# Kernel optimization log

Hardware: AMD Instinct MI355X
Metric: run time of the kernel (lower is better)

Reference implementation:

```python
import jax, jax.numpy as jnp
import numpy as np

EPS = 1e-5


def _rms_norm(x, w):
    # x: [..., C], w: [C]
    inv = jax.lax.rsqrt(jnp.mean(x * x, axis=-1, keepdims=True) + EPS)
    return x * inv * w


def setup_inputs() -> dict:
    key = jax.random.key(0)
    ks = jax.random.split(key, 8)
    N, H, C = 16384, 16, 32
    NE = 196608
    return {
        "q": jax.random.normal(ks[0], (N, H, C), dtype=jnp.float32),
        "k": jax.random.normal(ks[1], (N, H, C), dtype=jnp.float32),
        "v": jax.random.normal(ks[2], (N, H, C), dtype=jnp.float32),
        "e": jax.random.normal(ks[3], (NE, H, C), dtype=jnp.float32),
        "w_q_norm": jnp.ones((C,), dtype=jnp.float32),
        "w_k_norm": jnp.ones((C,), dtype=jnp.float32),
        "edge_src": jax.random.randint(ks[4], (NE,), 0, N, dtype=jnp.int32),
        "edge_dst": jax.random.randint(ks[5], (NE,), 0, N, dtype=jnp.int32),
    }


def reference(q, k, v, e, w_q_norm, w_k_norm, edge_src, edge_dst):
    N, H, C = q.shape
    qk_scale = 1.0 / np.sqrt(float(C))
    # fused QK RMSNorm (qk_norm == 1, elementwise_affine)
    qn = _rms_norm(q, w_q_norm)            # [N,H,C]
    kn = _rms_norm(k, w_k_norm)            # [N,H,C]
    ke = kn[edge_src] + e                  # [NE,H,C]
    ve = v[edge_src] + e                   # [NE,H,C]
    s = jnp.einsum("ehc,ehc->eh", qn[edge_dst], ke) * qk_scale  # [NE,H]
    # segment softmax over incoming edges per dst node
    m = jax.ops.segment_max(s, edge_dst, num_segments=N)        # [N,H]
    m = jnp.where(jnp.isfinite(m), m, 0.0)                      # empty rows -> 0 (matches kernel)
    alpha = jnp.exp(s - m[edge_dst])                            # [NE,H]
    denom = jax.ops.segment_sum(alpha, edge_dst, num_segments=N)            # [N,H]
    num = jax.ops.segment_sum(alpha[..., None] * ve, edge_dst, num_segments=N)  # [N,H,C]
    out = num / jnp.where(denom > 0, denom, 1.0)[..., None]
    return out
```

## Files before the change

kernel.cpp:

```cpp
#include <hip/hip_runtime.h>
#include <math.h>

#define H_DIM 16
#define C_DIM 32
#define HC_DIM (H_DIM * C_DIM)
#define EPSF 1e-5f

__device__ __forceinline__ float reduce8(float x) {
    x += __shfl_xor(x, 1);
    x += __shfl_xor(x, 2);
    x += __shfl_xor(x, 4);
    return x;
}

typedef float f4_raw __attribute__((ext_vector_type(4)));
__device__ __forceinline__ float4 nt_load4(const float* p) {
    f4_raw r = __builtin_nontemporal_load((const f4_raw*)p);
    return make_float4(r.x, r.y, r.z, r.w);
}
__device__ __forceinline__ void nt_store4(float* p, float4 v) {
    f4_raw r = {v.x, v.y, v.z, v.w};
    __builtin_nontemporal_store(r, (f4_raw*)p);
}

__global__ void zero_kernel(int* __restrict__ p, int n) {
    int i = blockIdx.x * blockDim.x + threadIdx.x;
    if (i < n) p[i] = 0;
}

__global__ void hist_kernel(const int* __restrict__ edst, int* __restrict__ counts, int ne) {
    int i = blockIdx.x * blockDim.x + threadIdx.x;
    if (i < ne) atomicAdd(&counts[edst[i]], 1);
}

__global__ void kinv_kernel(const float* __restrict__ k, float* __restrict__ kinv, int rows) {
    int gt = blockIdx.x * blockDim.x + threadIdx.x;
    int row = gt >> 3;
    if (row < rows) {
        const float4 kv = *(const float4*)(k + (size_t)row * C_DIM + ((gt & 7) << 2));
        float s = kv.x * kv.x + kv.y * kv.y + kv.z * kv.z + kv.w * kv.w;
        s = reduce8(s);
        if ((gt & 7) == 0) kinv[row] = rsqrtf(s * (1.0f / C_DIM) + EPSF);
    }
}

__global__ __launch_bounds__(1024)
void scan_kernel(const int* __restrict__ counts, int* __restrict__ offsets, int n) {
    __shared__ int wsum[16];
    __shared__ int carry_s;
    const int tid = threadIdx.x;
    const int lane = tid & 63;
    const int wid = tid >> 6;
    if (tid == 0) { carry_s = 0; offsets[0] = 0; }
    __syncthreads();
    for (int base = 0; base < n; base += 1024) {
        int x = (base + tid < n) ? counts[base + tid] : 0;
        int v = x;
        #pragma unroll
        for (int off = 1; off < 64; off <<= 1) {
            int y = __shfl_up(v, off);
            if (lane >= off) v += y;
        }
        if (lane == 63) wsum[wid] = v;
        __syncthreads();
        if (wid == 0 && lane < 16) {
            int s = wsum[lane];
            #pragma unroll
            for (int off = 1; off < 16; off <<= 1) {
                int y = __shfl_up(s, off);
                if (lane >= off) s += y;
            }
            wsum[lane] = s;
        }
        __syncthreads();
        int waveoff = (wid == 0) ? 0 : wsum[wid - 1];
        int carry = carry_s;
        if (base + tid < n) offsets[base + tid + 1] = carry + waveoff + v;
        __syncthreads();
        if (tid == 1023) carry_s = carry + wsum[15];
        __syncthreads();
    }
}

__global__ void scatter_kernel(const int* __restrict__ esrc, const int* __restrict__ edst,
                               const int* __restrict__ offsets, int* __restrict__ cursor,
                               int2* __restrict__ perm, int ne) {
    int i = blockIdx.x * blockDim.x + threadIdx.x;
    if (i < ne) {
        int d = edst[i];
        int pos = offsets[d] + atomicAdd(&cursor[d], 1);
        perm[pos] = make_int2(esrc[i], i);
    }
}

struct EdgeData {
    float4 ev, kv, vv;
    float  ki;
};

__device__ __forceinline__ EdgeData load_edge(int2 p,
                                              const float* __restrict__ e,
                                              const float* __restrict__ k,
                                              const float* __restrict__ v,
                                              const float* __restrict__ kinv,
                                              int hc, int h) {
    EdgeData d;
    d.ev = nt_load4(e + (size_t)p.y * HC_DIM + hc);
    d.kv = *(const float4*)(k + p.x * HC_DIM + hc);
    d.vv = *(const float4*)(v + p.x * HC_DIM + hc);
    d.ki = kinv[p.x * H_DIM + h];
    return d;
}

__device__ __forceinline__ void update_edge(const EdgeData& d,
                                            float4 qn, float4 wkv, float qk_scale,
                                            float& m, float& l, float4& acc) {
    float kex = d.kv.x * (d.ki * wkv.x) + d.ev.x;
    float key = d.kv.y * (d.ki * wkv.y) + d.ev.y;
    float kez = d.kv.z * (d.ki * wkv.z) + d.ev.z;
    float kew = d.kv.w * (d.ki * wkv.w) + d.ev.w;
    float dd = qn.x * kex + qn.y * key + qn.z * kez + qn.w * kew;
    dd = reduce8(dd);
    float s = dd * qk_scale;
    float mnew = fmaxf(m, s);
    float sc = __expf(m - mnew);
    float al = __expf(s - mnew);
    l = l * sc + al;
    acc.x = acc.x * sc + al * (d.vv.x + d.ev.x);
    acc.y = acc.y * sc + al * (d.vv.y + d.ev.y);
    acc.z = acc.z * sc + al * (d.vv.z + d.ev.z);
    acc.w = acc.w * sc + al * (d.vv.w + d.ev.w);
    m = mnew;
}

__global__ __launch_bounds__(128, 4)
void attn_kernel(const float* __restrict__ q, const float* __restrict__ k,
                 const float* __restrict__ v, const float* __restrict__ e,
                 const float* __restrict__ wq, const float* __restrict__ wk,
                 const float* __restrict__ kinv,
                 const int* __restrict__ offsets, const int2* __restrict__ perm,
                 float* __restrict__ out)
{
    const int node = blockIdx.x;
    const int t = threadIdx.x;
    const int hc = t << 2;
    const int c4 = (t & 7) << 2;
    const int h  = t >> 3;
    const float qk_scale = 0.17677669529663687f;

    const int node_off = node * HC_DIM + hc;

    float4 qv = *(const float4*)(q + node_off);
    float qs = qv.x * qv.x + qv.y * qv.y + qv.z * qv.z + qv.w * qv.w;
    qs = reduce8(qs);
    float qinv = rsqrtf(qs * (1.0f / C_DIM) + EPSF);
    float4 wqv = *(const float4*)(wq + c4);
    float4 qn = make_float4(qv.x * qinv * wqv.x, qv.y * qinv * wqv.y,
                            qv.z * qinv * wqv.z, qv.w * qinv * wqv.w);
    float4 wkv = *(const float4*)(wk + c4);

    const int row0 = offsets[node];
    const int row1 = offsets[node + 1];
    const int len = row1 - row0;
    const int mid = row0 + ((len + 1) >> 1);

    float mA = -INFINITY, lA = 0.0f, mB = -INFINITY, lB = 0.0f;
    float4 accA = make_float4(0.f, 0.f, 0.f, 0.f);
    float4 accB = make_float4(0.f, 0.f, 0.f, 0.f);

    int jA = row0, jB = mid;
    if (jB < row1) {
        int2 pA = perm[jA];
        int2 pB = perm[jB];
        EdgeData a = load_edge(pA, e, k, v, kinv, hc, h);
        EdgeData b = load_edge(pB, e, k, v, kinv, hc, h);
        ++jA; ++jB;
        bool haveNext = (jB < row1);
        int2 nA, nB;
        if (haveNext) { nA = perm[jA]; nB = perm[jB]; }
        while (haveNext) {
            EdgeData a2 = load_edge(nA, e, k, v, kinv, hc, h);
            EdgeData b2 = load_edge(nB, e, k, v, kinv, hc, h);
            ++jA; ++jB;
            haveNext = (jB < row1);
            if (haveNext) { nA = perm[jA]; nB = perm[jB]; }
            update_edge(a, qn, wkv, qk_scale, mA, lA, accA);
            update_edge(b, qn, wkv, qk_scale, mB, lB, accB);
            a = a2; b = b2;
        }
        update_edge(a, qn, wkv, qk_scale, mA, lA, accA);
        update_edge(b, qn, wkv, qk_scale, mB, lB, accB);
    }
    while (jA < mid) {
        int2 p = perm[jA];
        EdgeData a = load_edge(p, e, k, v, kinv, hc, h);
        update_edge(a, qn, wkv, qk_scale, mA, lA, accA);
        ++jA;
    }

    float M = fmaxf(mA, mB);
    float fA = (lA > 0.0f) ? __expf(mA - M) : 0.0f;
    float fB = (lB > 0.0f) ? __expf(mB - M) : 0.0f;
    float l = lA * fA + lB * fB;
    float4 acc = make_float4(accA.x * fA + accB.x * fB,
                             accA.y * fA + accB.y * fB,
                             accA.z * fA + accB.z * fB,
                             accA.w * fA + accB.w * fB);

    float invl = (l > 0.0f) ? (1.0f / l) : 0.0f;
    nt_store4(out + node_off, make_float4(acc.x * invl, acc.y * invl,
                                          acc.z * invl, acc.w * invl));
}

extern "C" void kernel_launch(void* const* d_in, const int* in_sizes, int n_in,
                              void* d_out, int out_size, void* d_ws, size_t ws_size,
                              hipStream_t stream) {
    const float* q  = (const float*)d_in[0];
    const float* k  = (const float*)d_in[1];
    const float* v  = (const float*)d_in[2];
    const float* e  = (const float*)d_in[3];
    const float* wq = (const float*)d_in[4];
    const float* wk = (const float*)d_in[5];
    const int* esrc = (const int*)d_in[6];
    const int* edst = (const int*)d_in[7];
    float* out = (float*)d_out;

    const int NE = in_sizes[6];
    const int HC = in_sizes[3] / NE;
    const int N  = in_sizes[0] / HC;

    int2* perm    = (int2*)d_ws;
    int* counts   = (int*)(perm + NE);
    int* cursor   = counts + N;
    int* offsets  = cursor + N;
    float* kinv   = (float*)(offsets + N + 1);

    const int rows = N * H_DIM;

    zero_kernel<<<(2 * N + 255) / 256, 256, 0, stream>>>(counts, 2 * N);
    hist_kernel<<<(NE + 255) / 256, 256, 0, stream>>>(edst, counts, NE);
    kinv_kernel<<<(rows * 8 + 255) / 256, 256, 0, stream>>>(k, kinv, rows);
    scan_kernel<<<1, 1024, 0, stream>>>(counts, offsets, N);
    scatter_kernel<<<(NE + 255) / 256, 256, 0, stream>>>(esrc, edst, offsets, cursor,
                                                         perm, NE);
    attn_kernel<<<N, 128, 0, stream>>>(q, k, v, e, wq, wk, kinv, offsets, perm, out);
}
```

Before: 696.4 us.

## Fuse histogram with k-norm, vectorize scan/scatter, fold scales into query

Merges the histogram and k-inverse-norm kernels into one launch and makes the histogram and scatter kernels handle four edges per thread with int4 loads. The scan now gives each thread 16 counts, cutting the loop to one iteration for 16384 nodes. In the attention kernel, the k-norm weight and qk scale are folded into precomputed query vectors, so each edge needs two dot products and no per-element key reconstruction. The q load is also marked nontemporal. The setup kernels are small next to the gather-bound attention kernel, so the combined effect is likely modest.

```diff
diff --git a/kernel.cpp b/kernel.cpp
--- a/kernel.cpp
+++ b/kernel.cpp
@@ -28,19 +28,30 @@
     if (i < n) p[i] = 0;
 }
 
-__global__ void hist_kernel(const int* __restrict__ edst, int* __restrict__ counts, int ne) {
-    int i = blockIdx.x * blockDim.x + threadIdx.x;
-    if (i < ne) atomicAdd(&counts[edst[i]], 1);
-}
-
-__global__ void kinv_kernel(const float* __restrict__ k, float* __restrict__ kinv, int rows) {
-    int gt = blockIdx.x * blockDim.x + threadIdx.x;
-    int row = gt >> 3;
-    if (row < rows) {
-        const float4 kv = *(const float4*)(k + (size_t)row * C_DIM + ((gt & 7) << 2));
-        float s = kv.x * kv.x + kv.y * kv.y + kv.z * kv.z + kv.w * kv.w;
-        s = reduce8(s);
-        if ((gt & 7) == 0) kinv[row] = rsqrtf(s * (1.0f / C_DIM) + EPSF);
+__global__ __launch_bounds__(256)
+void hist_kinv_kernel(const int* __restrict__ edst, int* __restrict__ counts,
+                      const float* __restrict__ k, float* __restrict__ kinv,
+                      int ne, int rows, int histBlocks) {
+    if ((int)blockIdx.x < histBlocks) {
+        int i4 = (blockIdx.x * 256 + threadIdx.x) * 4;
+        if (i4 + 4 <= ne) {
+            int4 d = *(const int4*)(edst + i4);
+            atomicAdd(&counts[d.x], 1);
+            atomicAdd(&counts[d.y], 1);
+            atomicAdd(&counts[d.z], 1);
+            atomicAdd(&counts[d.w], 1);
+        } else {
+            for (int j = i4; j < ne; ++j) atomicAdd(&counts[edst[j]], 1);
+        }
+    } else {
+        int gt = (blockIdx.x - histBlocks) * 256 + threadIdx.x;
+        int row = gt >> 3;
+        if (row < rows) {
+            const float4 kv = *(const float4*)(k + (size_t)row * C_DIM + ((gt & 7) << 2));
+            float s = kv.x * kv.x + kv.y * kv.y + kv.z * kv.z + kv.w * kv.w;
+            s = reduce8(s);
+            if ((gt & 7) == 0) kinv[row] = rsqrtf(s * (1.0f / C_DIM) + EPSF);
+        }
     }
 }
 
@@ -51,11 +62,26 @@
     const int tid = threadIdx.x;
     const int lane = tid & 63;
     const int wid = tid >> 6;
-    if (tid == 0) { carry_s = 0; offsets[0] = 0; }
+    if (tid == 0) carry_s = 0;
     __syncthreads();
-    for (int base = 0; base < n; base += 1024) {
-        int x = (base + tid < n) ? counts[base + tid] : 0;
-        int v = x;
+    for (int b0 = 0; b0 < n; b0 += 16384) {
+        const int base = b0 + tid * 16;
+        int c[16];
+        if (base + 16 <= n) {
+            const int4* p = (const int4*)(counts + base);
+            int4 t0 = p[0], t1 = p[1], t2 = p[2], t3 = p[3];
+            c[0]=t0.x; c[1]=t0.y; c[2]=t0.z; c[3]=t0.w;
+            c[4]=t1.x; c[5]=t1.y; c[6]=t1.z; c[7]=t1.w;
+            c[8]=t2.x; c[9]=t2.y; c[10]=t2.z; c[11]=t2.w;
+            c[12]=t3.x; c[13]=t3.y; c[14]=t3.z; c[15]=t3.w;
+        } else {
+            #pragma unroll
+            for (int j = 0; j < 16; ++j) c[j] = (base + j < n) ? counts[base + j] : 0;
+        }
+        int s = 0;
+        #pragma unroll
+        for (int j = 0; j < 16; ++j) s += c[j];
+        int v = s;
         #pragma unroll
         for (int off = 1; off < 64; off <<= 1) {
             int y = __shfl_up(v, off);
@@ -64,20 +90,34 @@
         if (lane == 63) wsum[wid] = v;
         __syncthreads();
         if (wid == 0 && lane < 16) {
-            int s = wsum[lane];
+            int w = wsum[lane];
             #pragma unroll
             for (int off = 1; off < 16; off <<= 1) {
-                int y = __shfl_up(s, off);
-                if (lane >= off) s += y;
+                int y = __shfl_up(w, off);
+                if (lane >= off) w += y;
             }
-            wsum[lane] = s;
+            wsum[lane] = w;
         }
         __syncthreads();
-        int waveoff = (wid == 0) ? 0 : wsum[wid - 1];
-        int carry = carry_s;
-        if (base + tid < n) offsets[base + tid + 1] = carry + waveoff + v;
+        const int carry = carry_s;
+        int p = carry + (wid ? wsum[wid - 1] : 0) + (v - s);
+        int o[16];
+        #pragma unroll
+        for (int j = 0; j < 16; ++j) { o[j] = p; p += c[j]; }
+        if (base + 16 <= n) {
+            int4* q = (int4*)(offsets + base);
+            q[0] = make_int4(o[0], o[1], o[2], o[3]);
+            q[1] = make_int4(o[4], o[5], o[6], o[7]);
+            q[2] = make_int4(o[8], o[9], o[10], o[11]);
+            q[3] = make_int4(o[12], o[13], o[14], o[15]);
+        } else {
+            #pragma unroll
+            for (int j = 0; j < 16; ++j)
+                if (base + j < n) offsets[base + j] = o[j];
+        }
+        if (n - 1 >= base && n - 1 < base + 16) offsets[n] = p;
         __syncthreads();
-        if (tid == 1023) carry_s = carry + wsum[15];
+        if (tid == 0) carry_s = carry + wsum[15];
         __syncthreads();
     }
 }
@@ -85,11 +125,24 @@
 __global__ void scatter_kernel(const int* __restrict__ esrc, const int* __restrict__ edst,
                                const int* __restrict__ offsets, int* __restrict__ cursor,
                                int2* __restrict__ perm, int ne) {
-    int i = blockIdx.x * blockDim.x + threadIdx.x;
-    if (i < ne) {
-        int d = edst[i];
-        int pos = offsets[d] + atomicAdd(&cursor[d], 1);
-        perm[pos] = make_int2(esrc[i], i);
+    int i4 = (blockIdx.x * blockDim.x + threadIdx.x) * 4;
+    if (i4 + 4 <= ne) {
+        int4 d = *(const int4*)(edst + i4);
+        int4 s = *(const int4*)(esrc + i4);
+        int p0 = offsets[d.x] + atomicAdd(&cursor[d.x], 1);
+        perm[p0] = make_int2(s.x, i4 + 0);
+        int p1 = offsets[d.y] + atomicAdd(&cursor[d.y], 1);
+        perm[p1] = make_int2(s.y, i4 + 1);
+        int p2 = offsets[d.z] + atomicAdd(&cursor[d.z], 1);
+        perm[p2] = make_int2(s.z, i4 + 2);
+        int p3 = offsets[d.w] + atomicAdd(&cursor[d.w], 1);
+        perm[p3] = make_int2(s.w, i4 + 3);
+    } else {
+        for (int j = i4; j < ne; ++j) {
+            int d = edst[j];
+            int pos = offsets[d] + atomicAdd(&cursor[d], 1);
+            perm[pos] = make_int2(esrc[j], j);
+        }
     }
 }
 
@@ -113,15 +166,11 @@
 }
 
 __device__ __forceinline__ void update_edge(const EdgeData& d,
-                                            float4 qn, float4 wkv, float qk_scale,
+                                            float4 qnw, float4 qns,
                                             float& m, float& l, float4& acc) {
-    float kex = d.kv.x * (d.ki * wkv.x) + d.ev.x;
-    float key = d.kv.y * (d.ki * wkv.y) + d.ev.y;
-    float kez = d.kv.z * (d.ki * wkv.z) + d.ev.z;
-    float kew = d.kv.w * (d.ki * wkv.w) + d.ev.w;
-    float dd = qn.x * kex + qn.y * key + qn.z * kez + qn.w * kew;
-    dd = reduce8(dd);
-    float s = dd * qk_scale;
+    float dk = qnw.x * d.kv.x + qnw.y * d.kv.y + qnw.z * d.kv.z + qnw.w * d.kv.w;
+    float de = qns.x * d.ev.x + qns.y * d.ev.y + qns.z * d.ev.z + qns.w * d.ev.w;
+    float s = reduce8(dk * d.ki + de);
     float mnew = fmaxf(m, s);
     float sc = __expf(m - mnew);
     float al = __expf(s - mnew);
@@ -150,14 +199,18 @@
 
     const int node_off = node * HC_DIM + hc;
 
-    float4 qv = *(const float4*)(q + node_off);
+    float4 qv = nt_load4(q + node_off);
     float qs = qv.x * qv.x + qv.y * qv.y + qv.z * qv.z + qv.w * qv.w;
     qs = reduce8(qs);
     float qinv = rsqrtf(qs * (1.0f / C_DIM) + EPSF);
     float4 wqv = *(const float4*)(wq + c4);
+    float4 wkv = *(const float4*)(wk + c4);
     float4 qn = make_float4(qv.x * qinv * wqv.x, qv.y * qinv * wqv.y,
                             qv.z * qinv * wqv.z, qv.w * qinv * wqv.w);
-    float4 wkv = *(const float4*)(wk + c4);
+    float4 qnw = make_float4(qn.x * wkv.x * qk_scale, qn.y * wkv.y * qk_scale,
+                             qn.z * wkv.z * qk_scale, qn.w * wkv.w * qk_scale);
+    float4 qns = make_float4(qn.x * qk_scale, qn.y * qk_scale,
+                             qn.z * qk_scale, qn.w * qk_scale);
 
     const int row0 = offsets[node];
     const int row1 = offsets[node + 1];
@@ -184,17 +237,17 @@
             ++jA; ++jB;
             haveNext = (jB < row1);
             if (haveNext) { nA = perm[jA]; nB = perm[jB]; }
-            update_edge(a, qn, wkv, qk_scale, mA, lA, accA);
-            update_edge(b, qn, wkv, qk_scale, mB, lB, accB);
+            update_edge(a, qnw, qns, mA, lA, accA);
+            update_edge(b, qnw, qns, mB, lB, accB);
             a = a2; b = b2;
         }
-        update_edge(a, qn, wkv, qk_scale, mA, lA, accA);
-        update_edge(b, qn, wkv, qk_scale, mB, lB, accB);
+        update_edge(a, qnw, qns, mA, lA, accA);
+        update_edge(b, qnw, qns, mB, lB, accB);
     }
     while (jA < mid) {
         int2 p = perm[jA];
         EdgeData a = load_edge(p, e, k, v, kinv, hc, h);
-        update_edge(a, qn, wkv, qk_scale, mA, lA, accA);
+        update_edge(a, qnw, qns, mA, lA, accA);
         ++jA;
     }
 
@@ -236,12 +289,15 @@
     float* kinv   = (float*)(offsets + N + 1);
 
     const int rows = N * H_DIM;
+    const int histBlocks = (NE / 4 + 255) / 256;
+    const int kinvBlocks = (rows * 8 + 255) / 256;
+    const int scatBlocks = (NE / 4 + 255) / 256;
 
     zero_kernel<<<(2 * N + 255) / 256, 256, 0, stream>>>(counts, 2 * N);
-    hist_kernel<<<(NE + 255) / 256, 256, 0, stream>>>(edst, counts, NE);
-    kinv_kernel<<<(rows * 8 + 255) / 256, 256, 0, stream>>>(k, kinv, rows);
+    hist_kinv_kernel<<<histBlocks + kinvBlocks, 256, 0, stream>>>(edst, counts, k, kinv,
+                                                                  NE, rows, histBlocks);
     scan_kernel<<<1, 1024, 0, stream>>>(counts, offsets, N);
-    scatter_kernel<<<(NE + 255) / 256, 256, 0, stream>>>(esrc, edst, offsets, cursor,
-                                                         perm, NE);
+    scatter_kernel<<<scatBlocks, 256, 0, stream>>>(esrc, edst, offsets, cursor,
+                                                   perm, NE);
     attn_kernel<<<N, 128, 0, stream>>>(q, k, v, e, wq, wk, kinv, offsets, perm, out);
 }
```

Result: no change. 685.9 us (-1.5%).
